# Optimization experiments

Hardware: AMD Instinct MI355X
Metric: run time of the kernel (lower is better)

## Reference

```python
import jax, jax.numpy as jnp
import numpy as np

B, L, HS = 32, 128, 512
P, M = 12, 1024
V, D = 50000, 128
P_TOTAL = 16
CHAR_LEN, CHAR_V = 16, 100
PRI_POS = (0, 1, 2, 3)  # privacy POS tags
TEMP = 1.0              # eval-mode temperature


def setup_inputs() -> dict:
    key = jax.random.key(0)
    ks = jax.random.split(key, 16)
    return {
        "ctx": jax.random.normal(ks[0], (B, L, HS), jnp.float32),
        "dec_W": jax.random.normal(ks[1], (P, HS, M), jnp.float32) * 0.05,
        "dec_b": jax.random.normal(ks[2], (P, M), jnp.float32) * 0.05,
        "psr_weight": jax.random.normal(ks[3], (V, D), jnp.float32),
        "atk_weight": jax.random.normal(ks[4], (V, D), jnp.float32),
        "cpy_W1": jax.random.normal(ks[5], (HS, 64), jnp.float32) * 0.05,
        "cpy_b1": jax.random.normal(ks[6], (64,), jnp.float32) * 0.05,
        "cpy_W2": jax.random.normal(ks[7], (64, 2), jnp.float32) * 0.05,
        "cpy_b2": jax.random.normal(ks[8], (2,), jnp.float32) * 0.05,
        "inp_word": jax.random.randint(ks[9], (B, L), 0, V),
        "inp_pos": jax.random.randint(ks[10], (B, L), 0, P_TOTAL),
        "inp_mask": jnp.ones((B, L), jnp.int32),
        "words": jax.random.randint(ks[11], (P, M), 0, V),
        "lut": jax.random.randint(ks[12], (V, CHAR_LEN), 0, CHAR_V),
    }


def _gumbel_softmax_hard(logits, key, t):
    # hard (straight-through) gumbel-softmax; forward value is one-hot
    u = jax.random.uniform(key, logits.shape, logits.dtype, 1e-6, 1.0 - 1e-6)
    g = -jnp.log(-jnp.log(u))
    y = jax.nn.softmax((logits + g) / t, axis=-1)
    idx = jnp.argmax(y, axis=-1)
    y_hard = jax.nn.one_hot(idx, logits.shape[-1], dtype=y.dtype)
    return y_hard + y - jax.lax.stop_gradient(y), idx


def reference(ctx, dec_W, dec_b, psr_weight, atk_weight,
              cpy_W1, cpy_b1, cpy_W2, cpy_b2,
              inp_word, inp_pos, inp_mask, words, lut):
    bs, ls = inp_word.shape
    N = bs * ls
    gkey = jax.random.key(42)

    ctx_f = ctx.reshape(N, -1)                      # [N, HS]
    pos_f = inp_pos.reshape(N)
    word_f = inp_word.reshape(N)

    ori_psr = psr_weight[word_f]                    # [N, D] gather
    ori_atk = atk_weight[word_f]
    obf_word = word_f
    obf_psr = ori_psr
    obf_atk = ori_atk
    obf_mask = jnp.zeros((N,), bool)
    pri_mask = jnp.zeros((N,), bool)
    entropy = jnp.float32(0.0)

    for p in range(P):  # small fixed set of POS tags (structurally distinct decoders)
        m = pos_f == p                              # [N] routing mask
        obf_mask = obf_mask | m
        if p in PRI_POS:
            pri_mask = pri_mask | m
        cnt = jnp.sum(m.astype(jnp.int32))
        logp = jax.nn.log_softmax(ctx_f @ dec_W[p] + dec_b[p], axis=-1)  # [N, M]
        ent_elem = -logp * jnp.exp(logp)
        ent_p = jnp.sum(jnp.where(m[:, None], ent_elem, 0.0)) / jnp.maximum(cnt * M, 1).astype(jnp.float32)
        entropy = entropy + jnp.where(cnt > 0, ent_p, 0.0)
        spt, idx = _gumbel_softmax_hard(logp, jax.random.fold_in(gkey, p), TEMP)
        spt_word = words[p][idx]                    # map local id -> vocab id
        obf_word = jnp.where(m, spt_word, obf_word)
        psr_p = spt @ psr_weight[words[p]]          # [N, D], per-POS sub-table
        atk_p = spt @ atk_weight[words[p]]
        obf_psr = jnp.where(m[:, None], psr_p, obf_psr)
        obf_atk = jnp.where(m[:, None], atk_p, obf_atk)

    # copy classifier
    h = jax.nn.relu(ctx_f @ cpy_W1 + cpy_b1)
    pcpy = jax.nn.log_softmax(h @ cpy_W2 + cpy_b2, axis=-1)  # [N, 2]
    # do_not_copy_pri: force pcpy to [0, 1] on privacy tokens
    pcpy = jnp.where(pri_mask[:, None], jnp.array([0.0, 1.0], pcpy.dtype), pcpy)

    cpy, _ = _gumbel_softmax_hard(pcpy, jax.random.fold_in(gkey, 999), TEMP)  # [N, 2]
    mask_f = inp_mask.reshape(N).astype(bool)
    cpy_mask = (cpy[:, 0] == 1.0) & mask_f

    noroot = inp_mask.astype(bool).at[:, 0].set(False).reshape(N)
    nr_cnt = jnp.maximum(jnp.sum(noroot.astype(jnp.int32)), 1).astype(jnp.float32)
    logp2 = jax.nn.log_softmax(pcpy, axis=-1)       # F.cross_entropy applies log_softmax again
    cpy_loss = -jnp.sum(jnp.where(noroot, logp2[:, 1], 0.0)) / nr_cnt  # cpy_penalty = 1.0 (applied twice)

    # use_copy: blend original vs obfuscated via (hard) copy gate
    c0, c1 = cpy[:, 0:1], cpy[:, 1:2]
    psr_out = (ori_psr * c0 + obf_psr * c1).reshape(bs, ls, -1)
    atk_out = (ori_atk * c0 + obf_atk * c1).reshape(bs, ls, -1)
    obf_mask = obf_mask & ~cpy_mask
    out_word = (word_f.astype(jnp.float32) * cpy[:, 0]
                + obf_word.astype(jnp.float32) * cpy[:, 1]).astype(jnp.int32).reshape(bs, ls)

    obf_char = lut[out_word]                        # [B, L, CHAR_LEN]
    ent_loss = -entropy  # ent_penalty = 1.0

    return (out_word, obf_char, psr_out, atk_out,
            obf_mask.reshape(bs, ls), cpy_mask.reshape(bs, ls),
            pri_mask.reshape(bs, ls), cpy_loss, ent_loss)
```

## Files before the change

kernel.cpp:

```cpp
#include <hip/hip_runtime.h>
#include <math.h>

#define BB 32
#define LL 128
#define HSZ 512
#define PP 12
#define MM 1024
#define VV 50000
#define DD 128
#define CLEN 16
#define NTOT 4096
#define LISTCAP 512

#define RT 64
#define CT 64
#define BK2 32
#define CPB 16

#define OFF_WORD  0
#define OFF_CHAR  4096
#define OFF_PSR   69632
#define OFF_ATK   593920
#define OFF_OBFM  1118208
#define OFF_CPYM  1122304
#define OFF_PRIM  1126400
#define OFF_CLOSS 1130496
#define OFF_ELOSS 1130497

#define WS_SC_OFF     6656
#define WS_LOGITS_OFF 16384

__device__ __forceinline__ float EXP32(float x){ return (float)exp((double)x); }
__device__ __forceinline__ float LOG32(float x){ return (float)log((double)x); }

__device__ __forceinline__ unsigned rotl32(unsigned x, int r){ return (x<<r)|(x>>(32-r)); }
__device__ __forceinline__ void tf2x32(unsigned k0, unsigned k1, unsigned x0, unsigned x1,
                                       unsigned &o0, unsigned &o1){
  unsigned ks2 = k0 ^ k1 ^ 0x1BD11BDAu;
  x0 += k0; x1 += k1;
  x0+=x1; x1=rotl32(x1,13); x1^=x0;
  x0+=x1; x1=rotl32(x1,15); x1^=x0;
  x0+=x1; x1=rotl32(x1,26); x1^=x0;
  x0+=x1; x1=rotl32(x1, 6); x1^=x0;
  x0+=k1; x1+=ks2+1u;
  x0+=x1; x1=rotl32(x1,17); x1^=x0;
  x0+=x1; x1=rotl32(x1,29); x1^=x0;
  x0+=x1; x1=rotl32(x1,16); x1^=x0;
  x0+=x1; x1=rotl32(x1,24); x1^=x0;
  x0+=ks2; x1+=k0+2u;
  x0+=x1; x1=rotl32(x1,13); x1^=x0;
  x0+=x1; x1=rotl32(x1,15); x1^=x0;
  x0+=x1; x1=rotl32(x1,26); x1^=x0;
  x0+=x1; x1=rotl32(x1, 6); x1^=x0;
  x0+=k0; x1+=k1+3u;
  x0+=x1; x1=rotl32(x1,17); x1^=x0;
  x0+=x1; x1=rotl32(x1,29); x1^=x0;
  x0+=x1; x1=rotl32(x1,16); x1^=x0;
  x0+=x1; x1=rotl32(x1,24); x1^=x0;
  x0+=k1; x1+=ks2+4u;
  x0+=x1; x1=rotl32(x1,13); x1^=x0;
  x0+=x1; x1=rotl32(x1,15); x1^=x0;
  x0+=x1; x1=rotl32(x1,26); x1^=x0;
  x0+=x1; x1=rotl32(x1, 6); x1^=x0;
  x0+=ks2; x1+=k0+5u;
  o0=x0; o1=x1;
}

__device__ __forceinline__ unsigned tf_bits32(unsigned k0, unsigned k1, unsigned e){
  unsigned o0, o1; tf2x32(k0, k1, 0u, e, o0, o1); return o0 ^ o1;
}

__device__ __forceinline__ float bits_to_unif(unsigned bits){
  const float lo = 1e-6f;
  const float hi = (float)(1.0 - 1e-6);
  const float span = hi - lo;
  unsigned fb = (bits >> 9) | 0x3f800000u;
  float f = __fsub_rn(__uint_as_float(fb), 1.0f);
  float r = __fadd_rn(__fmul_rn(f, span), lo);
  return fmaxf(lo, r);
}

__device__ __forceinline__ float gumbel_exact(unsigned bits){
  float u = bits_to_unif(bits);
  float v = -LOG32(u);
  return -LOG32(v);
}
__device__ __forceinline__ float gumbel_fast(unsigned bits){
  float u = bits_to_unif(bits);
  float v = -logf(u);
  return -logf(v);
}

__device__ __forceinline__ void gate_chain(int n, int pos, int msk,
                                           float p0f, float p1f,
                                           const float* __restrict__ cb2,
                                           float* __restrict__ sc0,
                                           float* __restrict__ sc1,
                                           float* __restrict__ closs)
{
  const bool ispri = (pos < 4);
  float pc0 = __fadd_rn(p0f, cb2[0]);
  float pc1 = __fadd_rn(p1f, cb2[1]);
  float m2  = fmaxf(pc0, pc1);
  float s0  = __fsub_rn(pc0, m2), s1 = __fsub_rn(pc1, m2);
  float se  = __fadd_rn(EXP32(s0), EXP32(s1));
  float lse = LOG32(se);
  float q0  = __fsub_rn(s0, lse), q1 = __fsub_rn(s1, lse);
  if (ispri){ q0 = 0.0f; q1 = 1.0f; }

  unsigned k90, k91; tf2x32(0u, 42u, 0u, 999u, k90, k91);
  float g0 = gumbel_exact(tf_bits32(k90, k91, (unsigned)(2*n)));
  float g1 = gumbel_exact(tf_bits32(k90, k91, (unsigned)(2*n + 1)));

  float x0 = __fadd_rn(q0, g0), x1 = __fadd_rn(q1, g1);
  float mmv = fmaxf(x0, x1);
  float ex0 = EXP32(__fsub_rn(x0, mmv));
  float ex1 = EXP32(__fsub_rn(x1, mmv));
  float ssum = __fadd_rn(ex0, ex1);
  float y0 = __fdiv_rn(ex0, ssum), y1 = __fdiv_rn(ex1, ssum);
  int   idx2 = (y1 > y0) ? 1 : 0;
  float ysel = idx2 ? y1 : y0;
  float c    = __fsub_rn(__fadd_rn(1.0f, ysel), ysel);
  *sc0 = (idx2 == 0) ? c : 0.0f;
  *sc1 = (idx2 == 1) ? c : 0.0f;

  float m3 = fmaxf(q0, q1);
  float t0 = __fsub_rn(q0, m3), t1 = __fsub_rn(q1, m3);
  float se2 = __fadd_rn(EXP32(t0), EXP32(t1));
  float l21 = __fsub_rn(t1, LOG32(se2));
  if (msk != 0 && (n & (LL-1)) != 0) atomicAdd(closs, l21);
}

__global__ __launch_bounds__(256)
void cpy_build_kernel(const float* __restrict__ ctx, const float* __restrict__ cW1,
                      const float* __restrict__ cb1, const float* __restrict__ cW2,
                      const float* __restrict__ cb2, const int* __restrict__ inp_pos,
                      const int* __restrict__ inp_mask, int* __restrict__ cntg,
                      int* __restrict__ rowlist, float* __restrict__ scbuf,
                      float* __restrict__ ws)
{
  const int n0 = blockIdx.x * CPB;
  const int t = threadIdx.x;

  if (t < CPB){
    int n = n0 + t;
    int p = inp_pos[n];
    if (p < PP){
      int slot = atomicAdd(&cntg[p], 1);
      if (slot < LISTCAP) rowlist[p*LISTCAP + slot] = n;
    }
  }

  __shared__ float W1s[64][68];
  __shared__ float Cs[CPB][68];

  const int r  = t >> 4;
  const int og = (t & 15) * 4;
  double acc[4] = {0.0, 0.0, 0.0, 0.0};

  for (int k0 = 0; k0 < HSZ; k0 += 64){
    #pragma unroll
    for (int i = 0; i < 4; ++i){
      int s = t + i*256;
      int kk = s >> 4, q = s & 15;
      float4 v = *(const float4*)(cW1 + (size_t)(k0+kk)*64 + q*4);
      *(float4*)&W1s[kk][q*4] = v;
    }
    {
      int rr = t >> 4, q = t & 15;
      float4 v = *(const float4*)(ctx + (size_t)(n0+rr)*HSZ + k0 + q*4);
      *(float4*)&Cs[rr][q*4] = v;
    }
    __syncthreads();
    #pragma unroll 4
    for (int kk = 0; kk < 64; ++kk){
      double c = (double)Cs[r][kk];
      acc[0] += c * (double)W1s[kk][og+0];
      acc[1] += c * (double)W1s[kk][og+1];
      acc[2] += c * (double)W1s[kk][og+2];
      acc[3] += c * (double)W1s[kk][og+3];
    }
    __syncthreads();
  }

  double p0 = 0.0, p1 = 0.0;
  #pragma unroll
  for (int j = 0; j < 4; ++j){
    float hv = __fadd_rn((float)acc[j], cb1[og+j]);
    hv = hv > 0.f ? hv : 0.f;
    double hd = (double)hv;
    p0 += hd * (double)cW2[2*(og+j)+0];
    p1 += hd * (double)cW2[2*(og+j)+1];
  }
  #pragma unroll
  for (int off = 1; off < 16; off <<= 1){
    p0 += __shfl_xor(p0, off);
    p1 += __shfl_xor(p1, off);
  }

  if ((t & 15) == 0){
    const int n = n0 + r;
    float c0v, c1v;
    gate_chain(n, inp_pos[n], inp_mask[n], (float)p0, (float)p1, cb2,
               &c0v, &c1v, ws + 12);
    scbuf[2*n + 0] = c0v;
    scbuf[2*n + 1] = c1v;
  }
}

__global__ __launch_bounds__(256)
void gemm_kernel(const float* __restrict__ ctx, const float* __restrict__ dec_W,
                 const int* __restrict__ cntg, const int* __restrict__ rowlist,
                 float* __restrict__ logits)
{
  const int p  = blockIdx.z;
  const int c0 = blockIdx.x * CT;
  const int r0 = blockIdx.y * RT;
  const int cnt0 = cntg[p];
  const int cnt  = cnt0 < LISTCAP ? cnt0 : LISTCAP;
  if (r0 >= cnt) return;
  const int t = threadIdx.x;

  __shared__ double As[RT][BK2+2];
  __shared__ double Bs[BK2][16][6];
  __shared__ int    rid_s[RT];

  if (t < RT){
    int rr = r0 + t;
    rid_s[t] = rowlist[p*LISTCAP + (rr < cnt ? rr : cnt-1)];
  }
  __syncthreads();

  const int tr = t >> 4, tc = t & 15;
  double acc[4][4];
  #pragma unroll
  for (int i = 0; i < 4; ++i)
    #pragma unroll
    for (int j = 0; j < 4; ++j) acc[i][j] = 0.0;

  const float* Wp = dec_W + (size_t)p * HSZ * MM;

  for (int k0 = 0; k0 < HSZ; k0 += BK2){
    #pragma unroll
    for (int i = 0; i < 2; ++i){
      int s = t + i*256;
      int rr = s >> 3, q = s & 7;
      float4 v = *(const float4*)(ctx + (size_t)rid_s[rr]*HSZ + k0 + q*4);
      double2 d0; d0.x = (double)v.x; d0.y = (double)v.y;
      double2 d1; d1.x = (double)v.z; d1.y = (double)v.w;
      *(double2*)&As[rr][q*4 + 0] = d0;
      *(double2*)&As[rr][q*4 + 2] = d1;
    }
    #pragma unroll
    for (int i = 0; i < 2; ++i){
      int s = t + i*256;
      int kk = s >> 4, q = s & 15;
      float4 v = *(const float4*)(Wp + (size_t)(k0+kk)*MM + c0 + q*4);
      double2 d0; d0.x = (double)v.x; d0.y = (double)v.y;
      double2 d1; d1.x = (double)v.z; d1.y = (double)v.w;
      *(double2*)&Bs[kk][q][0] = d0;
      *(double2*)&Bs[kk][q][2] = d1;
    }
    __syncthreads();
    #pragma unroll 4
    for (int kk = 0; kk < BK2; ++kk){
      double b0 = Bs[kk][tc][0];
      double b1 = Bs[kk][tc][1];
      double b2 = Bs[kk][tc][2];
      double b3 = Bs[kk][tc][3];
      double a0 = As[tr*4+0][kk];
      double a1 = As[tr*4+1][kk];
      double a2 = As[tr*4+2][kk];
      double a3 = As[tr*4+3][kk];
      acc[0][0]+=a0*b0; acc[0][1]+=a0*b1; acc[0][2]+=a0*b2; acc[0][3]+=a0*b3;
      acc[1][0]+=a1*b0; acc[1][1]+=a1*b1; acc[1][2]+=a1*b2; acc[1][3]+=a1*b3;
      acc[2][0]+=a2*b0; acc[2][1]+=a2*b1; acc[2][2]+=a2*b2; acc[2][3]+=a2*b3;
      acc[3][0]+=a3*b0; acc[3][1]+=a3*b1; acc[3][2]+=a3*b2; acc[3][3]+=a3*b3;
    }
    __syncthreads();
  }

  #pragma unroll
  for (int i = 0; i < 4; ++i){
    int rr = r0 + tr*4 + i;
    if (rr < cnt){
      int rg = rid_s[tr*4 + i];
      float4 o;
      o.x=(float)acc[i][0]; o.y=(float)acc[i][1]; o.z=(float)acc[i][2]; o.w=(float)acc[i][3];
      *(float4*)(logits + (size_t)rg*MM + c0 + tc*4) = o;
    }
  }
}

__global__ __launch_bounds__(256)
void finalize_kernel(const float* __restrict__ dec_b,
                     const float* __restrict__ psr_w, const float* __restrict__ atk_w,
                     const int* __restrict__ inp_word, const int* __restrict__ inp_pos,
                     const int* __restrict__ inp_mask, const int* __restrict__ words,
                     const int* __restrict__ lut, const float* __restrict__ logitsbuf,
                     const float* __restrict__ scbuf,
                     float* __restrict__ out, float* __restrict__ ws)
{
  const int wid = threadIdx.x >> 6, lane = threadIdx.x & 63;
  const int n = blockIdx.x * 4 + wid;

  const int  pos   = inp_pos[n];
  const int  word  = inp_word[n];
  const int  msk   = inp_mask[n];
  const bool isobf = (pos < PP);
  const bool ispri = (pos < 4);
  const float c0 = scbuf[2*n + 0];
  const float c1 = scbuf[2*n + 1];

  int bi = 0;
  if (isobf){
    float l[16];
    float lm = -3.4e38f;
    #pragma unroll
    for (int it = 0; it < 4; ++it){
      int m = it*256 + lane*4;
      float4 lg = *(const float4*)(logitsbuf + (size_t)n*MM + m);
      float4 bq = *(const float4*)(dec_b + (size_t)pos*MM + m);
      l[it*4+0] = __fadd_rn(lg.x, bq.x);
      l[it*4+1] = __fadd_rn(lg.y, bq.y);
      l[it*4+2] = __fadd_rn(lg.z, bq.z);
      l[it*4+3] = __fadd_rn(lg.w, bq.w);
      lm = fmaxf(lm, fmaxf(fmaxf(l[it*4+0], l[it*4+1]), fmaxf(l[it*4+2], l[it*4+3])));
    }
    #pragma unroll
    for (int off = 32; off > 0; off >>= 1) lm = fmaxf(lm, __shfl_xor(lm, off));
    const float xmax = lm;

    float e[16];
    double ds = 0.0;
    #pragma unroll
    for (int j = 0; j < 16; ++j){
      e[j] = expf(__fsub_rn(l[j], xmax));
      ds += (double)e[j];
    }
    #pragma unroll
    for (int off = 32; off > 0; off >>= 1) ds += __shfl_xor(ds, off);
    const double se = ds;
    const float lse = logf((float)se);
    const double inv_se = 1.0 / se;

    unsigned kp0, kp1; tf2x32(0u, 42u, 0u, (unsigned)pos, kp0, kp1);
    float best = -3.4e38f; double es = 0.0;
    #pragma unroll
    for (int it = 0; it < 4; ++it){
      #pragma unroll
      for (int j = 0; j < 4; ++j){
        int m = it*256 + lane*4 + j;
        float sh = __fsub_rn(l[it*4+j], xmax);
        float lp = __fsub_rn(sh, lse);
        es += (double)(-lp) * ((double)e[it*4+j] * inv_se);
        float g = gumbel_fast(tf_bits32(kp0, kp1, (unsigned)(n*MM + m)));
        float sv = __fadd_rn(lp, g);
        if (sv > best){ best = sv; bi = m; }
      }
    }
    #pragma unroll
    for (int off = 32; off > 0; off >>= 1){
      float ov = __shfl_xor(best, off);
      int   oi = __shfl_xor(bi,   off);
      if (ov > best || (ov == best && oi < bi)){ best = ov; bi = oi; }
      es += __shfl_xor(es, off);
    }
    if (lane == 0) atomicAdd(ws + pos, (float)es);
  }

  const int obf_word = isobf ? words[pos*MM + bi] : word;
  float of = __fadd_rn(__fmul_rn((float)word, c0), __fmul_rn((float)obf_word, c1));
  int ow = (int)of;
  if (lane == 0){
    out[OFF_WORD + n] = (float)ow;
    bool cpym = (c0 == 1.0f) && (msk != 0);
    out[OFF_CPYM + n] = cpym ? 1.f : 0.f;
    out[OFF_OBFM + n] = (isobf && !cpym) ? 1.f : 0.f;
    out[OFF_PRIM + n] = ispri ? 1.f : 0.f;
  }
  if (lane < CLEN)
    out[OFF_CHAR + (size_t)n*CLEN + lane] = (float)lut[(size_t)ow*CLEN + lane];
  #pragma unroll
  for (int rep = 0; rep < 2; ++rep){
    int j = lane + rep*64;
    float po = psr_w[(size_t)word*DD + j];
    float pb = isobf ? psr_w[(size_t)obf_word*DD + j] : po;
    out[OFF_PSR + (size_t)n*DD + j] = __fadd_rn(__fmul_rn(po, c0), __fmul_rn(pb, c1));
    float ao = atk_w[(size_t)word*DD + j];
    float ab = isobf ? atk_w[(size_t)obf_word*DD + j] : ao;
    out[OFF_ATK + (size_t)n*DD + j] = __fadd_rn(__fmul_rn(ao, c0), __fmul_rn(ab, c1));
  }
}

__global__ __launch_bounds__(256)
void fin_kernel(const int* __restrict__ inp_pos, const int* __restrict__ inp_mask,
                const float* __restrict__ ws, float* __restrict__ out)
{
  __shared__ int cnt[PP];
  __shared__ int nr;
  int t = threadIdx.x;
  if (t < PP) cnt[t] = 0;
  if (t == 0) nr = 0;
  __syncthreads();
  int ln = 0;
  for (int n = t; n < NTOT; n += 256){
    int p = inp_pos[n];
    if (p < PP) atomicAdd(&cnt[p], 1);
    if (inp_mask[n] != 0 && (n & (LL-1)) != 0) ln++;
  }
  atomicAdd(&nr, ln);
  __syncthreads();
  if (t == 0){
    float ent = 0.f;
    for (int p = 0; p < PP; ++p){
      int c = cnt[p];
      if (c > 0){
        int denom = c * MM; if (denom < 1) denom = 1;
        ent = __fadd_rn(ent, __fdiv_rn(ws[p], (float)denom));
      }
    }
    out[OFF_ELOSS] = -ent;
    int nrc = nr; if (nrc < 1) nrc = 1;
    out[OFF_CLOSS] = -__fdiv_rn(ws[12], (float)nrc);
  }
}

__global__ __launch_bounds__(256)
void row_kernel_mono(const float* __restrict__ ctx, const float* __restrict__ dec_W,
                const float* __restrict__ dec_b, const float* __restrict__ psr_w,
                const float* __restrict__ atk_w, const float* __restrict__ cW1,
                const float* __restrict__ cb1, const float* __restrict__ cW2,
                const float* __restrict__ cb2, const int* __restrict__ inp_word,
                const int* __restrict__ inp_pos, const int* __restrict__ inp_mask,
                const int* __restrict__ words, const int* __restrict__ lut,
                float* __restrict__ out, float* __restrict__ ws)
{
  const int n = blockIdx.x;
  const int t = threadIdx.x;

  __shared__ float  ctx_s[HSZ];
  __shared__ float  logit_s[MM];
  __shared__ float  h_s[64];
  __shared__ double redd[256];
  __shared__ float  redf[256];
  __shared__ int    redi[256];
  __shared__ float  sc[2];
  __shared__ int    si[1];

  for (int k = t; k < HSZ; k += 256) ctx_s[k] = ctx[(size_t)n*HSZ + k];
  __syncthreads();

  const int  pos   = inp_pos[n];
  const int  word  = inp_word[n];
  const int  msk   = inp_mask[n];
  const bool isobf = (pos < PP);
  const bool ispri = (pos < 4);

  if (t < 64){
    double acc = 0.0;
    for (int k = 0; k < HSZ; ++k) acc += (double)ctx_s[k] * (double)cW1[k*64 + t];
    float hv = __fadd_rn((float)acc, cb1[t]);
    h_s[t] = hv > 0.f ? hv : 0.f;
  }
  __syncthreads();

  if (t == 0){
    double a0 = 0.0, a1 = 0.0;
    for (int k = 0; k < 64; ++k){
      double hv = (double)h_s[k];
      a0 += hv * (double)cW2[k*2 + 0];
      a1 += hv * (double)cW2[k*2 + 1];
    }
    float c0v, c1v;
    gate_chain(n, pos, msk, (float)a0, (float)a1, cb2, &c0v, &c1v, ws + 12);
    sc[0] = c0v; sc[1] = c1v;
  }

  if (isobf){
    const float4* W4 = (const float4*)(dec_W + (size_t)pos * HSZ * MM);
    double a0=0.0, a1=0.0, a2=0.0, a3=0.0;
    for (int k = 0; k < HSZ; ++k){
      double c = (double)ctx_s[k];
      float4 w = W4[(size_t)k*256 + t];
      a0 += c*(double)w.x; a1 += c*(double)w.y; a2 += c*(double)w.z; a3 += c*(double)w.w;
    }
    const float* bp = dec_b + (size_t)pos * MM;
    const int m0 = 4*t;
    logit_s[m0+0] = __fadd_rn((float)a0, bp[m0+0]);
    logit_s[m0+1] = __fadd_rn((float)a1, bp[m0+1]);
    logit_s[m0+2] = __fadd_rn((float)a2, bp[m0+2]);
    logit_s[m0+3] = __fadd_rn((float)a3, bp[m0+3]);
    __syncthreads();

    float lm = logit_s[m0];
    lm = fmaxf(lm, logit_s[m0+1]); lm = fmaxf(lm, logit_s[m0+2]); lm = fmaxf(lm, logit_s[m0+3]);
    redf[t] = lm; __syncthreads();
    for (int s = 128; s > 0; s >>= 1){ if (t < s) redf[t] = fmaxf(redf[t], redf[t+s]); __syncthreads(); }
    const float xmax = redf[0];
    __syncthreads();

    double dsm = 0.0;
    for (int j = 0; j < 4; ++j)
      dsm += (double)EXP32(__fsub_rn(logit_s[m0+j], xmax));
    redd[t] = dsm; __syncthreads();
    for (int s = 128; s > 0; s >>= 1){ if (t < s) redd[t] += redd[t+s]; __syncthreads(); }
    const float lse = LOG32((float)redd[0]);
    __syncthreads();

    unsigned kp0, kp1; tf2x32(0u, 42u, 0u, (unsigned)pos, kp0, kp1);
    float best = -3.4e38f; int bi = 0; double es = 0.0;
    for (int j = 0; j < 4; ++j){
      int m = m0 + j;
      float sh = __fsub_rn(logit_s[m], xmax);
      float lp = __fsub_rn(sh, lse);
      float ex = EXP32(lp);
      es += (double)__fmul_rn(-lp, ex);
      float g = gumbel_exact(tf_bits32(kp0, kp1, (unsigned)(n*MM + m)));
      float sv = __fadd_rn(lp, g);
      if (sv > best){ best = sv; bi = m; }
    }
    redf[t] = best; redi[t] = bi; redd[t] = es; __syncthreads();
    for (int s = 128; s > 0; s >>= 1){
      if (t < s){
        float v2 = redf[t+s]; int i2 = redi[t+s];
        if (v2 > redf[t] || (v2 == redf[t] && i2 < redi[t])){ redf[t] = v2; redi[t] = i2; }
        redd[t] += redd[t+s];
      }
      __syncthreads();
    }
    if (t == 0){ si[0] = redi[0]; atomicAdd(ws + pos, (float)redd[0]); }
    __syncthreads();
  } else {
    __syncthreads();
  }

  const int   idx = isobf ? si[0] : 0;
  const float c0 = sc[0], c1 = sc[1];
  const int   obf_word = isobf ? words[pos*MM + idx] : word;

  if (t == 0){
    float of = __fadd_rn(__fmul_rn((float)word, c0), __fmul_rn((float)obf_word, c1));
    int ow = (int)of;
    out[OFF_WORD + n] = (float)ow;
    bool cpym = (c0 == 1.0f) && (msk != 0);
    out[OFF_CPYM + n] = cpym ? 1.f : 0.f;
    out[OFF_OBFM + n] = (isobf && !cpym) ? 1.f : 0.f;
    out[OFF_PRIM + n] = ispri ? 1.f : 0.f;
    #pragma unroll
    for (int j = 0; j < CLEN; ++j)
      out[OFF_CHAR + (size_t)n*CLEN + j] = (float)lut[(size_t)ow*CLEN + j];
  }
  if (t < DD){
    float po = psr_w[(size_t)word*DD + t];
    float pb = isobf ? psr_w[(size_t)obf_word*DD + t] : po;
    out[OFF_PSR + (size_t)n*DD + t] = __fadd_rn(__fmul_rn(po, c0), __fmul_rn(pb, c1));
    float ao = atk_w[(size_t)word*DD + t];
    float ab = isobf ? atk_w[(size_t)obf_word*DD + t] : ao;
    out[OFF_ATK + (size_t)n*DD + t] = __fadd_rn(__fmul_rn(ao, c0), __fmul_rn(ab, c1));
  }
}

extern "C" void kernel_launch(void* const* d_in, const int* in_sizes, int n_in,
                              void* d_out, int out_size, void* d_ws, size_t ws_size,
                              hipStream_t stream)
{
  const float* ctx      = (const float*)d_in[0];
  const float* dec_W    = (const float*)d_in[1];
  const float* dec_b    = (const float*)d_in[2];
  const float* psr_w    = (const float*)d_in[3];
  const float* atk_w    = (const float*)d_in[4];
  const float* cW1      = (const float*)d_in[5];
  const float* cb1      = (const float*)d_in[6];
  const float* cW2      = (const float*)d_in[7];
  const float* cb2      = (const float*)d_in[8];
  const int*   inp_word = (const int*)d_in[9];
  const int*   inp_pos  = (const int*)d_in[10];
  const int*   inp_mask = (const int*)d_in[11];
  const int*   words    = (const int*)d_in[12];
  const int*   lut      = (const int*)d_in[13];
  float* out = (float*)d_out;
  float* ws  = (float*)d_ws;

  const size_t need = ((size_t)WS_LOGITS_OFF + (size_t)NTOT*MM) * 4;

  hipMemsetAsync(ws, 0, 512, stream);

  if (ws_size >= need){
    int*   cntg      = (int*)ws + 16;
    int*   rowlist   = (int*)ws + 64;
    float* scbuf     = ws + WS_SC_OFF;
    float* logitsbuf = ws + WS_LOGITS_OFF;
    cpy_build_kernel<<<NTOT/CPB, 256, 0, stream>>>(ctx, cW1, cb1, cW2, cb2,
                                                   inp_pos, inp_mask, cntg, rowlist,
                                                   scbuf, ws);
    gemm_kernel<<<dim3(MM/CT, LISTCAP/RT, PP), 256, 0, stream>>>(ctx, dec_W, cntg,
                                                                 rowlist, logitsbuf);
    finalize_kernel<<<NTOT/4, 256, 0, stream>>>(dec_b, psr_w, atk_w,
                                                inp_word, inp_pos, inp_mask, words, lut,
                                                logitsbuf, scbuf, out, ws);
  } else {
    row_kernel_mono<<<NTOT, 256, 0, stream>>>(ctx, dec_W, dec_b, psr_w, atk_w,
                                              cW1, cb1, cW2, cb2,
                                              inp_word, inp_pos, inp_mask, words, lut,
                                              out, ws);
  }
  fin_kernel<<<1, 256, 0, stream>>>(inp_pos, inp_mask, ws, out);
}
```

Before: 325.7 us.

## Replace atomic bucketing and loss accumulation with deterministic ballot scan and reduction kernel

Moves row bucketing by POS into a dedicated kernel that uses wave ballots and prefix counts instead of global atomics, giving a stable row order. The per-position entropy and copy-loss atomics are replaced with per-row stores (the entropy is stashed in the logits buffer) and a single-block reduction kernel. The workspace memset is removed from the fast path. This adds one extra small launch and a serial scan over tokens in exchange for removing atomic contention and nondeterministic ordering.

```diff
diff --git a/kernel.cpp b/kernel.cpp
--- a/kernel.cpp
+++ b/kernel.cpp
@@ -91,12 +91,11 @@
   return -logf(v);
 }
 
-__device__ __forceinline__ void gate_chain(int n, int pos, int msk,
+__device__ __forceinline__ void gate_chain(int n, int pos,
                                            float p0f, float p1f,
                                            const float* __restrict__ cb2,
-                                           float* __restrict__ sc0,
-                                           float* __restrict__ sc1,
-                                           float* __restrict__ closs)
+                                           float* __restrict__ sc_enc,
+                                           float* __restrict__ l21_out)
 {
   const bool ispri = (pos < 4);
   float pc0 = __fadd_rn(p0f, cb2[0]);
@@ -121,35 +120,56 @@
   int   idx2 = (y1 > y0) ? 1 : 0;
   float ysel = idx2 ? y1 : y0;
   float c    = __fsub_rn(__fadd_rn(1.0f, ysel), ysel);
-  *sc0 = (idx2 == 0) ? c : 0.0f;
-  *sc1 = (idx2 == 1) ? c : 0.0f;
+  *sc_enc = idx2 ? c : -c;
 
   float m3 = fmaxf(q0, q1);
   float t0 = __fsub_rn(q0, m3), t1 = __fsub_rn(q1, m3);
   float se2 = __fadd_rn(EXP32(t0), EXP32(t1));
-  float l21 = __fsub_rn(t1, LOG32(se2));
-  if (msk != 0 && (n & (LL-1)) != 0) atomicAdd(closs, l21);
+  *l21_out = __fsub_rn(t1, LOG32(se2));
+}
+
+__global__ __launch_bounds__(256)
+void bucket_kernel(const int* __restrict__ inp_pos, int* __restrict__ cntg,
+                   int* __restrict__ rowlist)
+{
+  const int p = blockIdx.x;
+  const int t = threadIdx.x;
+  const int w = t >> 6, lane = t & 63;
+  __shared__ int wtot[4];
+  __shared__ int base_s;
+  if (t == 0) base_s = 0;
+  __syncthreads();
+  for (int n0 = 0; n0 < NTOT; n0 += 256){
+    int n = n0 + t;
+    int m = (inp_pos[n] == p) ? 1 : 0;
+    unsigned long long bal = __ballot(m);
+    int excl = __popcll(bal & ((1ULL << lane) - 1ULL));
+    if (lane == 0) wtot[w] = __popcll(bal);
+    __syncthreads();
+    int wbase = 0;
+    #pragma unroll
+    for (int i = 0; i < 4; ++i) if (i < w) wbase += wtot[i];
+    int tot = wtot[0] + wtot[1] + wtot[2] + wtot[3];
+    int b = base_s;
+    if (m){
+      int slot = b + wbase + excl;
+      if (slot < LISTCAP) rowlist[p*LISTCAP + slot] = n;
+    }
+    __syncthreads();
+    if (t == 0) base_s = b + tot;
+    __syncthreads();
+  }
+  if (t == 0) cntg[p] = base_s;
 }
 
 __global__ __launch_bounds__(256)
 void cpy_build_kernel(const float* __restrict__ ctx, const float* __restrict__ cW1,
                       const float* __restrict__ cb1, const float* __restrict__ cW2,
                       const float* __restrict__ cb2, const int* __restrict__ inp_pos,
-                      const int* __restrict__ inp_mask, int* __restrict__ cntg,
-                      int* __restrict__ rowlist, float* __restrict__ scbuf,
-                      float* __restrict__ ws)
+                      float* __restrict__ scbuf)
 {
   const int n0 = blockIdx.x * CPB;
   const int t = threadIdx.x;
-
-  if (t < CPB){
-    int n = n0 + t;
-    int p = inp_pos[n];
-    if (p < PP){
-      int slot = atomicAdd(&cntg[p], 1);
-      if (slot < LISTCAP) rowlist[p*LISTCAP + slot] = n;
-    }
-  }
 
   __shared__ float W1s[64][68];
   __shared__ float Cs[CPB][68];
@@ -200,11 +220,10 @@
 
   if ((t & 15) == 0){
     const int n = n0 + r;
-    float c0v, c1v;
-    gate_chain(n, inp_pos[n], inp_mask[n], (float)p0, (float)p1, cb2,
-               &c0v, &c1v, ws + 12);
-    scbuf[2*n + 0] = c0v;
-    scbuf[2*n + 1] = c1v;
+    float senc, l21;
+    gate_chain(n, inp_pos[n], (float)p0, (float)p1, cb2, &senc, &l21);
+    scbuf[2*n + 0] = senc;
+    scbuf[2*n + 1] = l21;
   }
 }
 
@@ -297,9 +316,9 @@
                      const float* __restrict__ psr_w, const float* __restrict__ atk_w,
                      const int* __restrict__ inp_word, const int* __restrict__ inp_pos,
                      const int* __restrict__ inp_mask, const int* __restrict__ words,
-                     const int* __restrict__ lut, const float* __restrict__ logitsbuf,
+                     const int* __restrict__ lut, float* __restrict__ logitsbuf,
                      const float* __restrict__ scbuf,
-                     float* __restrict__ out, float* __restrict__ ws)
+                     float* __restrict__ out)
 {
   const int wid = threadIdx.x >> 6, lane = threadIdx.x & 63;
   const int n = blockIdx.x * 4 + wid;
@@ -309,8 +328,9 @@
   const int  msk   = inp_mask[n];
   const bool isobf = (pos < PP);
   const bool ispri = (pos < 4);
-  const float c0 = scbuf[2*n + 0];
-  const float c1 = scbuf[2*n + 1];
+  const float senc = scbuf[2*n + 0];
+  const float c0 = (senc < 0.f) ? -senc : 0.f;
+  const float c1 = (senc < 0.f) ? 0.f : senc;
 
   int bi = 0;
   if (isobf){
@@ -366,7 +386,9 @@
       if (ov > best || (ov == best && oi < bi)){ best = ov; bi = oi; }
       es += __shfl_xor(es, off);
     }
-    if (lane == 0) atomicAdd(ws + pos, (float)es);
+    if (lane == 0) logitsbuf[(size_t)n*MM] = (float)es;
+  } else {
+    if (lane == 0) logitsbuf[(size_t)n*MM] = 0.f;
   }
 
   const int obf_word = isobf ? words[pos*MM + bi] : word;
@@ -393,6 +415,64 @@
   }
 }
 
+__global__ __launch_bounds__(1024)
+void fin2_kernel(const int* __restrict__ inp_pos, const int* __restrict__ inp_mask,
+                 const float* __restrict__ scbuf, const float* __restrict__ logitsbuf,
+                 float* __restrict__ out)
+{
+  const int t = threadIdx.x;
+  const int w = t >> 6, lane = t & 63;
+  __shared__ double s_ent[PP];
+  __shared__ int    s_cnt[PP];
+  __shared__ double s_cl;
+  __shared__ int    s_nr;
+
+  if (w < PP){
+    const int p = w;
+    double es = 0.0; int c = 0;
+    for (int n = lane; n < NTOT; n += 64){
+      if (inp_pos[n] == p){
+        es += (double)logitsbuf[(size_t)n*MM];
+        c  += 1;
+      }
+    }
+    #pragma unroll
+    for (int off = 1; off < 64; off <<= 1){
+      es += __shfl_xor(es, off);
+      c  += __shfl_xor(c, off);
+    }
+    if (lane == 0){ s_ent[p] = es; s_cnt[p] = c; }
+  } else if (w == PP){
+    double cl = 0.0; int nr = 0;
+    for (int n = lane; n < NTOT; n += 64){
+      if (inp_mask[n] != 0 && (n & (LL-1)) != 0){
+        cl += (double)scbuf[2*n + 1];
+        nr += 1;
+      }
+    }
+    #pragma unroll
+    for (int off = 1; off < 64; off <<= 1){
+      cl += __shfl_xor(cl, off);
+      nr += __shfl_xor(nr, off);
+    }
+    if (lane == 0){ s_cl = cl; s_nr = nr; }
+  }
+  __syncthreads();
+  if (t == 0){
+    float ent = 0.f;
+    for (int p = 0; p < PP; ++p){
+      int c = s_cnt[p];
+      if (c > 0){
+        int denom = c * MM; if (denom < 1) denom = 1;
+        ent = __fadd_rn(ent, __fdiv_rn((float)s_ent[p], (float)denom));
+      }
+    }
+    out[OFF_ELOSS] = -ent;
+    int nrc = s_nr; if (nrc < 1) nrc = 1;
+    out[OFF_CLOSS] = -__fdiv_rn((float)s_cl, (float)nrc);
+  }
+}
+
 __global__ __launch_bounds__(256)
 void fin_kernel(const int* __restrict__ inp_pos, const int* __restrict__ inp_mask,
                 const float* __restrict__ ws, float* __restrict__ out)
@@ -472,9 +552,11 @@
       a0 += hv * (double)cW2[k*2 + 0];
       a1 += hv * (double)cW2[k*2 + 1];
     }
-    float c0v, c1v;
-    gate_chain(n, pos, msk, (float)a0, (float)a1, cb2, &c0v, &c1v, ws + 12);
-    sc[0] = c0v; sc[1] = c1v;
+    float senc, l21;
+    gate_chain(n, pos, (float)a0, (float)a1, cb2, &senc, &l21);
+    sc[0] = (senc < 0.f) ? -senc : 0.f;
+    sc[1] = (senc < 0.f) ? 0.f : senc;
+    if (msk != 0 && (n & (LL-1)) != 0) atomicAdd(ws + 12, l21);
   }
 
   if (isobf){
@@ -584,26 +666,26 @@
 
   const size_t need = ((size_t)WS_LOGITS_OFF + (size_t)NTOT*MM) * 4;
 
-  hipMemsetAsync(ws, 0, 512, stream);
-
   if (ws_size >= need){
     int*   cntg      = (int*)ws + 16;
     int*   rowlist   = (int*)ws + 64;
     float* scbuf     = ws + WS_SC_OFF;
     float* logitsbuf = ws + WS_LOGITS_OFF;
+    bucket_kernel<<<PP, 256, 0, stream>>>(inp_pos, cntg, rowlist);
     cpy_build_kernel<<<NTOT/CPB, 256, 0, stream>>>(ctx, cW1, cb1, cW2, cb2,
-                                                   inp_pos, inp_mask, cntg, rowlist,
-                                                   scbuf, ws);
+                                                   inp_pos, scbuf);
     gemm_kernel<<<dim3(MM/CT, LISTCAP/RT, PP), 256, 0, stream>>>(ctx, dec_W, cntg,
                                                                  rowlist, logitsbuf);
     finalize_kernel<<<NTOT/4, 256, 0, stream>>>(dec_b, psr_w, atk_w,
                                                 inp_word, inp_pos, inp_mask, words, lut,
-                                                logitsbuf, scbuf, out, ws);
+                                                logitsbuf, scbuf, out);
+    fin2_kernel<<<1, 1024, 0, stream>>>(inp_pos, inp_mask, scbuf, logitsbuf, out);
   } else {
+    hipMemsetAsync(ws, 0, 512, stream);
     row_kernel_mono<<<NTOT, 256, 0, stream>>>(ctx, dec_W, dec_b, psr_w, atk_w,
                                               cW1, cb1, cW2, cb2,
                                               inp_word, inp_pos, inp_mask, words, lut,
                                               out, ws);
-  }
-  fin_kernel<<<1, 256, 0, stream>>>(inp_pos, inp_mask, ws, out);
-}
+    fin_kernel<<<1, 256, 0, stream>>>(inp_pos, inp_mask, ws, out);
+  }
+}
```

After: 322.6 us. About the same (-0.9%).
